# Kernel tuning notes

Hardware: AMD Instinct MI355X
Metric: run time of the kernel (lower is better)

The kernel has to match this reference:

```python
import jax, jax.numpy as jnp
import numpy as np

N, D, E = 16384, 256, 131072  # nodes, feature dim, directed edges (avg sym degree ~16)


def _build_graph(rng):
    # random edges with no self-loops
    r = rng.integers(0, N, E)
    c = (r + 1 + rng.integers(0, N - 1, E)) % N
    e = np.stack([r, c], 1)
    # symmetrize + dedupe + sort == torch sparse coalesce()
    e = np.unique(np.concatenate([e, e[:, ::-1]], 0), axis=0)
    rows, cols = e[:, 0], e[:, 1]
    deg = np.bincount(rows, minlength=N)
    max_deg = int(deg.max())
    off = np.concatenate([[0], np.cumsum(deg)])
    pos = np.arange(rows.shape[0]) - off[rows]
    nbr = np.zeros((N, max_deg), dtype=np.int32)  # padded neighbor lists (CSR rows)
    nbr[rows, pos] = cols
    return nbr, deg.astype(np.int32)


def setup_inputs() -> dict:
    rng = np.random.default_rng(0)
    vertices = jnp.asarray(rng.standard_normal((N, D)).astype(np.float32))
    nbr, deg = _build_graph(rng)
    return {"vertices": vertices, "nbr": jnp.asarray(nbr), "deg": jnp.asarray(deg)}


def _compute_means(vertices, nbr, deg):
    # Sequential greedy edge-based vertex averaging (RelEdgePool phase 1).
    n, d = vertices.shape
    max_deg = nbr.shape[1]
    slot = jnp.arange(max_deg)

    def step(carry, xs):
        unproc, out, c = carry
        i, nbrs_i, deg_i = xs
        valid = slot < deg_i                      # real (non-pad) neighbors
        sel = valid & unproc[nbrs_i]              # unprocessed cluster members (excl. self)
        is_head = unproc[i]                       # vertex starts a new valid cluster
        # mean over unprocessed members; self is always included when head
        s = jnp.einsum('kd,k->d', vertices[nbrs_i], sel.astype(vertices.dtype)) + vertices[i]
        cnt = (jnp.sum(sel) + 1).astype(vertices.dtype)
        mean = s / cnt
        out = out.at[c].set(jnp.where(is_head, mean, out[c]))
        # mark selected members (and self) as processed, only if this is a head
        mark = jnp.zeros(n, bool).at[nbrs_i].max(sel).at[i].set(True)
        unproc = unproc & ~(mark & is_head)
        c = c + is_head.astype(c.dtype)
        return (unproc, out, c), is_head

    init = (jnp.ones(n, dtype=bool), jnp.zeros((n, d), vertices.dtype), jnp.int32(0))
    (_, out, num_clusters), head_mask = jax.lax.scan(
        step, init, (jnp.arange(n), nbr, deg))
    # out[:num_clusters] are the averaged vertices; rows beyond are zero (preallocated buffer,
    # matching the torch code before its final data-dependent slice).
    # head_mask marks vertex_mappings; mean_mappings == arange(num_clusters).
    return out, head_mask, num_clusters


def reference(vertices, nbr, deg):
    return _compute_means(vertices, nbr, deg)
```

## Files before the change

### kernel.cpp

```cpp
#include <hip/hip_runtime.h>
#include <cstdint>
#include <cstddef>

#define NV 16384
#define DD 256
#define TPB 1024
#define BLK 2048
#define PCAP 7
#define HROW 24
#define NPASS 12

#define CFENCE() asm volatile("" ::: "memory")

__global__ __launch_bounds__(256)
void k_prep(const int* __restrict__ nbr, const int* __restrict__ deg,
            int maxdeg, int n, uint4* __restrict__ pend_g,
            unsigned short* __restrict__ hi_g)
{
    int v = blockIdx.x * 256 + threadIdx.x;
    if (v >= n) return;
    const int b  = v & ~(BLK - 1);
    const int dv = deg[v];
    const int* __restrict__ row = nbr + (size_t)v * (size_t)maxdeg;
    unsigned short* __restrict__ hrow = hi_g + (size_t)v * HROW;
    unsigned w0 = 0, w1 = 0, w2 = 0, w3 = 0;
    int cnt = 0, hic = 0;
    for (int k = 0; k < dv; ++k) {
        int j = row[k];
        if (j > v) {
            if (hic < HROW - 1) hrow[1 + hic] = (unsigned short)j;
            ++hic;
        } else if (j >= b) {
            unsigned val = (unsigned)(j - b);
            switch (cnt) {
                case 0: w0 |= val << 16; break;
                case 1: w1 |= val;       break;
                case 2: w1 |= val << 16; break;
                case 3: w2 |= val;       break;
                case 4: w2 |= val << 16; break;
                case 5: w3 |= val;       break;
                case 6: w3 |= val << 16; break;
                default: break;
            }
            ++cnt;
        }
    }
    hrow[0] = (unsigned short)hic;
    w0 |= (unsigned)(cnt > 0xffff ? 0xffff : cnt);
    pend_g[v] = make_uint4(w0, w1, w2, w3);
}

__device__ __forceinline__
void do_push(unsigned char* st, int V,
             const unsigned short* __restrict__ hi_g,
             const int* __restrict__ nbr, const int* __restrict__ deg,
             int maxdeg)
{
    const uint4* hp = (const uint4*)(hi_g + (size_t)V * HROW);
    uint4 H0 = hp[0], H1 = hp[1], H2 = hp[2];
    const int hic = (int)(H0.x & 0xffffu);
    if (hic <= HROW - 1) {
        #define PUSHE(word, sh, k) if ((k) < hic) st[((word) >> (sh)) & 0xffffu] = 2
        PUSHE(H0.x,16, 0); PUSHE(H0.y, 0, 1); PUSHE(H0.y,16, 2);
        PUSHE(H0.z, 0, 3); PUSHE(H0.z,16, 4); PUSHE(H0.w, 0, 5);
        PUSHE(H0.w,16, 6);
        PUSHE(H1.x, 0, 7); PUSHE(H1.x,16, 8); PUSHE(H1.y, 0, 9);
        PUSHE(H1.y,16,10); PUSHE(H1.z, 0,11); PUSHE(H1.z,16,12);
        PUSHE(H1.w, 0,13); PUSHE(H1.w,16,14);
        PUSHE(H2.x, 0,15); PUSHE(H2.x,16,16); PUSHE(H2.y, 0,17);
        PUSHE(H2.y,16,18); PUSHE(H2.z, 0,19); PUSHE(H2.z,16,20);
        PUSHE(H2.w, 0,21); PUSHE(H2.w,16,22);
        #undef PUSHE
    } else {
        const int dv = deg[V];
        const int* __restrict__ row = nbr + (size_t)V * (size_t)maxdeg;
        for (int k = 0; k < dv; ++k) {
            int j = row[k];
            if (j > V) st[j] = 2;
        }
    }
}

__device__ __forceinline__
void decide(int& my, unsigned char* st, int V, int np, int qown,
            int q0, int q1, int q2, int q3, int q4, int q5, int q6, int B,
            const unsigned short* __restrict__ hi_g,
            const int* __restrict__ nbr, const int* __restrict__ deg,
            int maxdeg)
{
    if (qown != 0) { my = 2; return; }
    bool anyH = false; int undec = 0;
    if (np <= PCAP) {
        if (np > 0) { anyH |= (q0 == 1); undec += (q0 == 0); }
        if (np > 1) { anyH |= (q1 == 1); undec += (q1 == 0); }
        if (np > 2) { anyH |= (q2 == 1); undec += (q2 == 0); }
        if (np > 3) { anyH |= (q3 == 1); undec += (q3 == 0); }
        if (np > 4) { anyH |= (q4 == 1); undec += (q4 == 0); }
        if (np > 5) { anyH |= (q5 == 1); undec += (q5 == 0); }
        if (np > 6) { anyH |= (q6 == 1); undec += (q6 == 0); }
    } else {
        const int dv = deg[V];
        const int* __restrict__ row = nbr + (size_t)V * (size_t)maxdeg;
        for (int k = 0; k < dv; ++k) {
            int j = row[k];
            if (j >= B && j < V) {
                int q = st[j];
                anyH |= (q == 1); undec += (q == 0);
            }
        }
    }
    if (anyH) { my = 2; st[V] = 2; }
    else if (undec == 0) {
        my = 1; st[V] = 1;
        do_push(st, V, hi_g, nbr, deg, maxdeg);
    }
}

__global__ __launch_bounds__(TPB, 4)
void k_mis(const int* __restrict__ nbr, const int* __restrict__ deg,
           int maxdeg, int n,
           const uint4* __restrict__ pend_g, const unsigned short* __restrict__ hi_g,
           int* __restrict__ headlist, float* __restrict__ out_tail)
{
    __shared__ __align__(16) unsigned char st[NV];
    __shared__ int s_ws[TPB / 64];
    __shared__ int F[3];
    const int t    = threadIdx.x;
    const int lane = t & 63;
    const int wid  = t >> 6;

    ((uint4*)st)[t] = make_uint4(0u, 0u, 0u, 0u);
    if (t < 3) F[t] = 0;
    __syncthreads();

    uint4 pa0 = make_uint4(0,0,0,0), pa1 = pa0;
    if (t < n)        pa0 = pend_g[t];
    if (1024 + t < n) pa1 = pend_g[1024 + t];
    int r = 0;

    for (int b = 0; b < n; b += BLK) {
        const int v0 = b + t, v1 = b + 1024 + t;
        uint4 qa0 = make_uint4(0,0,0,0), qa1 = qa0;
        {
            int w0 = b + BLK + t, w1 = b + BLK + 1024 + t;
            if (w0 < n) qa0 = pend_g[w0];
            if (w1 < n) qa1 = pend_g[w1];
        }

        const int np0 = pa0.x & 0xffff;
        const int e0 = pa0.x >> 16,    e1 = pa0.y & 0xffff, e2 = pa0.y >> 16;
        const int e3 = pa0.z & 0xffff, e4 = pa0.z >> 16;
        const int e5 = pa0.w & 0xffff, e6 = pa0.w >> 16;
        const int np1 = pa1.x & 0xffff;
        const int f0 = pa1.x >> 16,    f1 = pa1.y & 0xffff, f2 = pa1.y >> 16;
        const int f3 = pa1.z & 0xffff, f4 = pa1.z >> 16;
        const int f5 = pa1.w & 0xffff, f6 = pa1.w >> 16;

        int my0 = (v0 < n) ? 0 : 2;
        int my1 = (v1 < n) ? 0 : 2;

        for (;; ++r) {
            if (t == 0) F[(r + 1) % 3] = 0;
            for (int pass = 0; pass < NPASS; ++pass) {
                int s0  = st[v0 < n ? v0 : 0],  s1  = st[v1 < n ? v1 : 0];
                int q00 = st[b + e0], q01 = st[b + e1], q02 = st[b + e2];
                int q03 = st[b + e3], q04 = st[b + e4], q05 = st[b + e5];
                int q06 = st[b + e6];
                int q10 = st[b + f0], q11 = st[b + f1], q12 = st[b + f2];
                int q13 = st[b + f3], q14 = st[b + f4], q15 = st[b + f5];
                int q16 = st[b + f6];
                if (my0 == 0) decide(my0, st, v0, np0, s0,
                                     q00,q01,q02,q03,q04,q05,q06, b,
                                     hi_g, nbr, deg, maxdeg);
                if (my1 == 0) decide(my1, st, v1, np1, s1,
                                     q10,q11,q12,q13,q14,q15,q16, b,
                                     hi_g, nbr, deg, maxdeg);
                if (__ballot((my0 == 0) || (my1 == 0)) == 0ULL) break;
                CFENCE();
            }
            if ((my0 == 0) || (my1 == 0)) F[r % 3] = 1;
            asm volatile("s_waitcnt lgkmcnt(0)\n\ts_barrier" ::: "memory");
            if (F[r % 3] == 0) { ++r; break; }
        }
        pa0 = qa0; pa1 = qa1;
    }

    uint4 qq = ((const uint4*)st)[t];
    int cnt = __popc(qq.x & 0x01010101u) + __popc(qq.y & 0x01010101u)
            + __popc(qq.z & 0x01010101u) + __popc(qq.w & 0x01010101u);
    int c = cnt;
    #pragma unroll
    for (int off = 1; off < 64; off <<= 1) {
        int x = __shfl_up(c, off);
        if (lane >= off) c += x;
    }
    if (lane == 63) s_ws[wid] = c;
    __syncthreads();
    int wexcl = 0, tot = 0;
    #pragma unroll
    for (int w = 0; w < TPB / 64; ++w) {
        int s = s_ws[w];
        tot += s;
        if (w < wid) wexcl += s;
    }
    int excl = wexcl + (c - cnt);
    #pragma unroll
    for (int i = 0; i < 16; ++i) {
        int v = t * 16 + i;
        if (st[v] == 1) { headlist[excl] = v; ++excl; }
    }
    for (int i = t; i < NV / 4; i += TPB) {
        unsigned w = ((const unsigned*)st)[i];
        float4 f;
        f.x = (float)(w & 1u);         f.y = (float)((w >> 8) & 1u);
        f.z = (float)((w >> 16) & 1u); f.w = (float)((w >> 24) & 1u);
        ((float4*)out_tail)[i] = f;
    }
    if (t == 0) out_tail[n] = (float)tot;
}

__global__ __launch_bounds__(256)
void k_avg(const float* __restrict__ vert, const int* __restrict__ nbr,
           const int* __restrict__ deg, int maxdeg, int n,
           const int* __restrict__ headlist,
           const float* __restrict__ tail, float* __restrict__ out)
{
    const int w    = (blockIdx.x * 256 + threadIdx.x) >> 6;
    const int lane = threadIdx.x & 63;
    if (w >= n) return;
    const int tot  = (int)tail[n];
    if (w >= tot) {
        reinterpret_cast<float4*>(out + (size_t)w * DD)[lane] = make_float4(0.f, 0.f, 0.f, 0.f);
        return;
    }
    const int h = headlist[w];

    const int dh = deg[h];
    const int* __restrict__ row = nbr + (size_t)h * (size_t)maxdeg;

    float4 acc = reinterpret_cast<const float4*>(vert + (size_t)h * DD)[lane];
    int cnt = 1;

    for (int k0 = 0; k0 < dh; k0 += 64) {
        int k = k0 + lane;
        int j = (k < dh) ? row[k] : -1;
        bool mem = false;
        if (j > h && tail[j] == 0.0f) {
            const int dj = deg[j];
            const int* __restrict__ rj = nbr + (size_t)j * (size_t)maxdeg;
            int mn = 0x7fffffff;
            for (int kk = 0; kk < dj; ++kk) {
                int u = rj[kk];
                if (tail[u] != 0.0f) mn = min(mn, u);
            }
            mem = (mn == h);
        }
        unsigned long long m = __ballot(mem);
        cnt += __popcll(m);
        while (m) {
            int bit = __ffsll((long long)m) - 1;
            m &= (m - 1);
            int jj = __shfl(j, bit);
            float4 rr = reinterpret_cast<const float4*>(vert + (size_t)jj * DD)[lane];
            acc.x += rr.x; acc.y += rr.y; acc.z += rr.z; acc.w += rr.w;
        }
    }
    const float inv = 1.0f / (float)cnt;
    float4 res;
    res.x = acc.x * inv; res.y = acc.y * inv;
    res.z = acc.z * inv; res.w = acc.w * inv;
    reinterpret_cast<float4*>(out + (size_t)w * DD)[lane] = res;
}

extern "C" void kernel_launch(void* const* d_in, const int* in_sizes, int n_in,
                              void* d_out, int out_size, void* d_ws, size_t ws_size,
                              hipStream_t stream)
{
    const float* vert = (const float*)d_in[0];
    const int*   nbr  = (const int*)d_in[1];
    const int*   deg  = (const int*)d_in[2];

    const int n      = in_sizes[2];
    const int maxdeg = in_sizes[1] / n;
    const int d      = in_sizes[0] / n;

    int*   headlist = (int*)d_ws;
    uint4* pend_g   = (uint4*)(headlist + n);
    unsigned short* hi_g = (unsigned short*)(pend_g + n);

    float* out      = (float*)d_out;
    float* out_tail = out + (size_t)n * (size_t)d;

    hipLaunchKernelGGL(k_prep, dim3((n + 255) / 256), dim3(256), 0, stream,
                       nbr, deg, maxdeg, n, pend_g, hi_g);

    hipLaunchKernelGGL(k_mis, dim3(1), dim3(TPB), 0, stream,
                       nbr, deg, maxdeg, n, pend_g, hi_g, headlist, out_tail);

    const int blocks = (n * 64 + 255) / 256;
    hipLaunchKernelGGL(k_avg, dim3(blocks), dim3(256), 0, stream,
                       vert, nbr, deg, maxdeg, n, headlist, out_tail, out);
}
```

Before: 87.38 us.

## Replace push-based neighbor marking with pull-based check of earlier-block heads

Heads no longer push a 'covered' mark to their higher-index neighbours. Instead, each vertex pulls at the start of its block: it checks whether any lower-index neighbour from an earlier block is already a head, using packed neighbour lists of up to 23 entries prepared in k_prep. This removes scattered shared-memory writes and the per-head global reads of the hi list from the serial in-block iteration loop. In exchange it adds more register state per thread (three extra uint4 per vertex) and reduces the pass count from 12 to 10.

```diff
diff --git a/kernel.cpp b/kernel.cpp
--- a/kernel.cpp
+++ b/kernel.cpp
@@ -6,91 +6,117 @@
 #define DD 256
 #define TPB 1024
 #define BLK 2048
+#define OCAP 23
 #define PCAP 7
-#define HROW 24
-#define NPASS 12
+#define NPASS 10
 
 #define CFENCE() asm volatile("" ::: "memory")
 
 __global__ __launch_bounds__(256)
 void k_prep(const int* __restrict__ nbr, const int* __restrict__ deg,
-            int maxdeg, int n, uint4* __restrict__ pend_g,
-            unsigned short* __restrict__ hi_g)
+            int maxdeg, int n, uint4* __restrict__ old_g,
+            uint4* __restrict__ pend_g)
 {
     int v = blockIdx.x * 256 + threadIdx.x;
     if (v >= n) return;
-    const int b  = v & ~(BLK - 1);
+    const int B  = v & ~(BLK - 1);
     const int dv = deg[v];
     const int* __restrict__ row = nbr + (size_t)v * (size_t)maxdeg;
-    unsigned short* __restrict__ hrow = hi_g + (size_t)v * HROW;
-    unsigned w0 = 0, w1 = 0, w2 = 0, w3 = 0;
-    int cnt = 0, hic = 0;
+    unsigned o0=0,o1=0,o2=0,o3=0,o4=0,o5=0,o6=0,o7=0,o8=0,o9=0,o10=0,o11=0;
+    unsigned w0=0,w1=0,w2=0,w3=0;
+    int no = 0, np = 0;
     for (int k = 0; k < dv; ++k) {
         int j = row[k];
-        if (j > v) {
-            if (hic < HROW - 1) hrow[1 + hic] = (unsigned short)j;
-            ++hic;
-        } else if (j >= b) {
-            unsigned val = (unsigned)(j - b);
-            switch (cnt) {
-                case 0: w0 |= val << 16; break;
-                case 1: w1 |= val;       break;
-                case 2: w1 |= val << 16; break;
-                case 3: w2 |= val;       break;
-                case 4: w2 |= val << 16; break;
-                case 5: w3 |= val;       break;
-                case 6: w3 |= val << 16; break;
+        if (j >= v) continue;
+        if (j < B) {
+            unsigned e = (unsigned)j;
+            switch (no) {
+                case 0:  o0 |= e << 16; break;
+                case 1:  o1 |= e; break;      case 2:  o1 |= e << 16; break;
+                case 3:  o2 |= e; break;      case 4:  o2 |= e << 16; break;
+                case 5:  o3 |= e; break;      case 6:  o3 |= e << 16; break;
+                case 7:  o4 |= e; break;      case 8:  o4 |= e << 16; break;
+                case 9:  o5 |= e; break;      case 10: o5 |= e << 16; break;
+                case 11: o6 |= e; break;      case 12: o6 |= e << 16; break;
+                case 13: o7 |= e; break;      case 14: o7 |= e << 16; break;
+                case 15: o8 |= e; break;      case 16: o8 |= e << 16; break;
+                case 17: o9 |= e; break;      case 18: o9 |= e << 16; break;
+                case 19: o10 |= e; break;     case 20: o10 |= e << 16; break;
+                case 21: o11 |= e; break;     case 22: o11 |= e << 16; break;
                 default: break;
             }
-            ++cnt;
-        }
-    }
-    hrow[0] = (unsigned short)hic;
-    w0 |= (unsigned)(cnt > 0xffff ? 0xffff : cnt);
+            ++no;
+        } else {
+            unsigned e = (unsigned)(j - B);
+            switch (np) {
+                case 0: w0 |= e << 16; break;
+                case 1: w1 |= e; break;  case 2: w1 |= e << 16; break;
+                case 3: w2 |= e; break;  case 4: w2 |= e << 16; break;
+                case 5: w3 |= e; break;  case 6: w3 |= e << 16; break;
+                default: break;
+            }
+            ++np;
+        }
+    }
+    o0 |= (unsigned)(no > 0xffff ? 0xffff : no);
+    w0 |= (unsigned)(np > 0xffff ? 0xffff : np);
+    old_g[3 * (size_t)v]     = make_uint4(o0, o1, o2, o3);
+    old_g[3 * (size_t)v + 1] = make_uint4(o4, o5, o6, o7);
+    old_g[3 * (size_t)v + 2] = make_uint4(o8, o9, o10, o11);
     pend_g[v] = make_uint4(w0, w1, w2, w3);
 }
 
 __device__ __forceinline__
-void do_push(unsigned char* st, int V,
-             const unsigned short* __restrict__ hi_g,
-             const int* __restrict__ nbr, const int* __restrict__ deg,
-             int maxdeg)
-{
-    const uint4* hp = (const uint4*)(hi_g + (size_t)V * HROW);
-    uint4 H0 = hp[0], H1 = hp[1], H2 = hp[2];
-    const int hic = (int)(H0.x & 0xffffu);
-    if (hic <= HROW - 1) {
-        #define PUSHE(word, sh, k) if ((k) < hic) st[((word) >> (sh)) & 0xffffu] = 2
-        PUSHE(H0.x,16, 0); PUSHE(H0.y, 0, 1); PUSHE(H0.y,16, 2);
-        PUSHE(H0.z, 0, 3); PUSHE(H0.z,16, 4); PUSHE(H0.w, 0, 5);
-        PUSHE(H0.w,16, 6);
-        PUSHE(H1.x, 0, 7); PUSHE(H1.x,16, 8); PUSHE(H1.y, 0, 9);
-        PUSHE(H1.y,16,10); PUSHE(H1.z, 0,11); PUSHE(H1.z,16,12);
-        PUSHE(H1.w, 0,13); PUSHE(H1.w,16,14);
-        PUSHE(H2.x, 0,15); PUSHE(H2.x,16,16); PUSHE(H2.y, 0,17);
-        PUSHE(H2.y,16,18); PUSHE(H2.z, 0,19); PUSHE(H2.z,16,20);
-        PUSHE(H2.w, 0,21); PUSHE(H2.w,16,22);
-        #undef PUSHE
-    } else {
+bool any_old_head(const unsigned char* st, uint4 A, uint4 Bw, uint4 Cw, int no,
+                  int V, int B, const int* __restrict__ nbr,
+                  const int* __restrict__ deg, int maxdeg)
+{
+    if (no > OCAP) {
         const int dv = deg[V];
         const int* __restrict__ row = nbr + (size_t)V * (size_t)maxdeg;
-        for (int k = 0; k < dv; ++k) {
-            int j = row[k];
-            if (j > V) st[j] = 2;
-        }
-    }
+        bool a = false;
+        for (int k = 0; k < dv; ++k) { int j = row[k]; if (j < B) a |= (st[j] == 1); }
+        return a;
+    }
+    bool a;
+    {
+        int q0 = st[A.x >> 16],      q1 = st[A.y & 0xffffu], q2 = st[A.y >> 16];
+        int q3 = st[A.z & 0xffffu],  q4 = st[A.z >> 16],     q5 = st[A.w & 0xffffu];
+        int q6 = st[A.w >> 16],      q7 = st[Bw.x & 0xffffu];
+        a = (no > 0 && q0 == 1) || (no > 1 && q1 == 1) || (no > 2 && q2 == 1)
+         || (no > 3 && q3 == 1) || (no > 4 && q4 == 1) || (no > 5 && q5 == 1)
+         || (no > 6 && q6 == 1) || (no > 7 && q7 == 1);
+    }
+    if (no > 8) {
+        int q8  = st[Bw.x >> 16],     q9  = st[Bw.y & 0xffffu], q10 = st[Bw.y >> 16];
+        int q11 = st[Bw.z & 0xffffu], q12 = st[Bw.z >> 16],     q13 = st[Bw.w & 0xffffu];
+        int q14 = st[Bw.w >> 16],     q15 = st[Cw.x & 0xffffu];
+        a = a || (q8 == 1) || (no > 9 && q9 == 1) || (no > 10 && q10 == 1)
+              || (no > 11 && q11 == 1) || (no > 12 && q12 == 1)
+              || (no > 13 && q13 == 1) || (no > 14 && q14 == 1)
+              || (no > 15 && q15 == 1);
+    }
+    if (no > 16) {
+        int q16 = st[Cw.x >> 16],     q17 = st[Cw.y & 0xffffu], q18 = st[Cw.y >> 16];
+        int q19 = st[Cw.z & 0xffffu], q20 = st[Cw.z >> 16],     q21 = st[Cw.w & 0xffffu];
+        int q22 = st[Cw.w >> 16];
+        a = a || (q16 == 1) || (no > 17 && q17 == 1) || (no > 18 && q18 == 1)
+              || (no > 19 && q19 == 1) || (no > 20 && q20 == 1)
+              || (no > 21 && q21 == 1) || (no > 22 && q22 == 1);
+    }
+    return a;
 }
 
 __device__ __forceinline__
-void decide(int& my, unsigned char* st, int V, int np, int qown,
-            int q0, int q1, int q2, int q3, int q4, int q5, int q6, int B,
-            const unsigned short* __restrict__ hi_g,
-            const int* __restrict__ nbr, const int* __restrict__ deg,
-            int maxdeg)
-{
-    if (qown != 0) { my = 2; return; }
+void pend_decide(int& my, unsigned char* st, int V, int B, uint4 P, int np,
+                 int dvf, const int* __restrict__ nbr, int maxdeg)
+{
     bool anyH = false; int undec = 0;
     if (np <= PCAP) {
+        int q0 = st[B + (P.x >> 16)],      q1 = st[B + (P.y & 0xffffu)];
+        int q2 = st[B + (P.y >> 16)],      q3 = st[B + (P.z & 0xffffu)];
+        int q4 = st[B + (P.z >> 16)],      q5 = st[B + (P.w & 0xffffu)];
+        int q6 = st[B + (P.w >> 16)];
         if (np > 0) { anyH |= (q0 == 1); undec += (q0 == 0); }
         if (np > 1) { anyH |= (q1 == 1); undec += (q1 == 0); }
         if (np > 2) { anyH |= (q2 == 1); undec += (q2 == 0); }
@@ -99,27 +125,20 @@
         if (np > 5) { anyH |= (q5 == 1); undec += (q5 == 0); }
         if (np > 6) { anyH |= (q6 == 1); undec += (q6 == 0); }
     } else {
-        const int dv = deg[V];
         const int* __restrict__ row = nbr + (size_t)V * (size_t)maxdeg;
-        for (int k = 0; k < dv; ++k) {
+        for (int k = 0; k < dvf; ++k) {
             int j = row[k];
-            if (j >= B && j < V) {
-                int q = st[j];
-                anyH |= (q == 1); undec += (q == 0);
-            }
-        }
-    }
-    if (anyH) { my = 2; st[V] = 2; }
-    else if (undec == 0) {
-        my = 1; st[V] = 1;
-        do_push(st, V, hi_g, nbr, deg, maxdeg);
-    }
+            if (j >= B && j < V) { int q = st[j]; anyH |= (q == 1); undec += (q == 0); }
+        }
+    }
+    if (anyH)            { my = 2; st[V] = 2; }
+    else if (undec == 0) { my = 1; st[V] = 1; }
 }
 
 __global__ __launch_bounds__(TPB, 4)
 void k_mis(const int* __restrict__ nbr, const int* __restrict__ deg,
            int maxdeg, int n,
-           const uint4* __restrict__ pend_g, const unsigned short* __restrict__ hi_g,
+           const uint4* __restrict__ old_g, const uint4* __restrict__ pend_g,
            int* __restrict__ headlist, float* __restrict__ out_tail)
 {
     __shared__ __align__(16) unsigned char st[NV];
@@ -133,48 +152,62 @@
     if (t < 3) F[t] = 0;
     __syncthreads();
 
-    uint4 pa0 = make_uint4(0,0,0,0), pa1 = pa0;
-    if (t < n)        pa0 = pend_g[t];
-    if (1024 + t < n) pa1 = pend_g[1024 + t];
+    uint4 a0A = make_uint4(0,0,0,0), a0B = a0A, a0C = a0A, p0 = a0A;
+    uint4 a1A = a0A, a1B = a0A, a1C = a0A, p1 = a0A;
+    {
+        int v0 = t, v1 = 1024 + t;
+        if (v0 < n) {
+            a0A = old_g[3*(size_t)v0]; a0B = old_g[3*(size_t)v0+1];
+            a0C = old_g[3*(size_t)v0+2]; p0 = pend_g[v0];
+        }
+        if (v1 < n) {
+            a1A = old_g[3*(size_t)v1]; a1B = old_g[3*(size_t)v1+1];
+            a1C = old_g[3*(size_t)v1+2]; p1 = pend_g[v1];
+        }
+    }
     int r = 0;
 
     for (int b = 0; b < n; b += BLK) {
         const int v0 = b + t, v1 = b + 1024 + t;
-        uint4 qa0 = make_uint4(0,0,0,0), qa1 = qa0;
+        uint4 s0A = make_uint4(0,0,0,0), s0B = s0A, s0C = s0A, q0 = s0A;
+        uint4 s1A = s0A, s1B = s0A, s1C = s0A, q1 = s0A;
         {
             int w0 = b + BLK + t, w1 = b + BLK + 1024 + t;
-            if (w0 < n) qa0 = pend_g[w0];
-            if (w1 < n) qa1 = pend_g[w1];
-        }
-
-        const int np0 = pa0.x & 0xffff;
-        const int e0 = pa0.x >> 16,    e1 = pa0.y & 0xffff, e2 = pa0.y >> 16;
-        const int e3 = pa0.z & 0xffff, e4 = pa0.z >> 16;
-        const int e5 = pa0.w & 0xffff, e6 = pa0.w >> 16;
-        const int np1 = pa1.x & 0xffff;
-        const int f0 = pa1.x >> 16,    f1 = pa1.y & 0xffff, f2 = pa1.y >> 16;
-        const int f3 = pa1.z & 0xffff, f4 = pa1.z >> 16;
-        const int f5 = pa1.w & 0xffff, f6 = pa1.w >> 16;
+            if (w0 < n) {
+                s0A = old_g[3*(size_t)w0]; s0B = old_g[3*(size_t)w0+1];
+                s0C = old_g[3*(size_t)w0+2]; q0 = pend_g[w0];
+            }
+            if (w1 < n) {
+                s1A = old_g[3*(size_t)w1]; s1B = old_g[3*(size_t)w1+1];
+                s1C = old_g[3*(size_t)w1+2]; q1 = pend_g[w1];
+            }
+        }
+
+        const int no0 = (int)(a0A.x & 0xffffu), np0 = (int)(p0.x & 0xffffu);
+        const int no1 = (int)(a1A.x & 0xffffu), np1 = (int)(p1.x & 0xffffu);
 
         int my0 = (v0 < n) ? 0 : 2;
         int my1 = (v1 < n) ? 0 : 2;
+        int dvf0 = 0, dvf1 = 0;
+        if (my0 == 0 && np0 > PCAP) dvf0 = deg[v0];
+        if (my1 == 0 && np1 > PCAP) dvf1 = deg[v1];
+
+        if (my0 == 0) {
+            bool aH = any_old_head(st, a0A, a0B, a0C, no0, v0, b, nbr, deg, maxdeg);
+            if (aH)            { my0 = 2; st[v0] = 2; }
+            else if (np0 == 0) { my0 = 1; st[v0] = 1; }
+        }
+        if (my1 == 0) {
+            bool aH = any_old_head(st, a1A, a1B, a1C, no1, v1, b, nbr, deg, maxdeg);
+            if (aH)            { my1 = 2; st[v1] = 2; }
+            else if (np1 == 0) { my1 = 1; st[v1] = 1; }
+        }
 
         for (;; ++r) {
             if (t == 0) F[(r + 1) % 3] = 0;
             for (int pass = 0; pass < NPASS; ++pass) {
-                int s0  = st[v0 < n ? v0 : 0],  s1  = st[v1 < n ? v1 : 0];
-                int q00 = st[b + e0], q01 = st[b + e1], q02 = st[b + e2];
-                int q03 = st[b + e3], q04 = st[b + e4], q05 = st[b + e5];
-                int q06 = st[b + e6];
-                int q10 = st[b + f0], q11 = st[b + f1], q12 = st[b + f2];
-                int q13 = st[b + f3], q14 = st[b + f4], q15 = st[b + f5];
-                int q16 = st[b + f6];
-                if (my0 == 0) decide(my0, st, v0, np0, s0,
-                                     q00,q01,q02,q03,q04,q05,q06, b,
-                                     hi_g, nbr, deg, maxdeg);
-                if (my1 == 0) decide(my1, st, v1, np1, s1,
-                                     q10,q11,q12,q13,q14,q15,q16, b,
-                                     hi_g, nbr, deg, maxdeg);
+                if (my0 == 0) pend_decide(my0, st, v0, b, p0, np0, dvf0, nbr, maxdeg);
+                if (my1 == 0) pend_decide(my1, st, v1, b, p1, np1, dvf1, nbr, maxdeg);
                 if (__ballot((my0 == 0) || (my1 == 0)) == 0ULL) break;
                 CFENCE();
             }
@@ -182,7 +215,8 @@
             asm volatile("s_waitcnt lgkmcnt(0)\n\ts_barrier" ::: "memory");
             if (F[r % 3] == 0) { ++r; break; }
         }
-        pa0 = qa0; pa1 = qa1;
+        a0A = s0A; a0B = s0B; a0C = s0C; p0 = q0;
+        a1A = s1A; a1B = s1B; a1C = s1C; p1 = q1;
     }
 
     uint4 qq = ((const uint4*)st)[t];
@@ -286,16 +320,16 @@
 
     int*   headlist = (int*)d_ws;
     uint4* pend_g   = (uint4*)(headlist + n);
-    unsigned short* hi_g = (unsigned short*)(pend_g + n);
+    uint4* old_g    = pend_g + n;
 
     float* out      = (float*)d_out;
     float* out_tail = out + (size_t)n * (size_t)d;
 
     hipLaunchKernelGGL(k_prep, dim3((n + 255) / 256), dim3(256), 0, stream,
-                       nbr, deg, maxdeg, n, pend_g, hi_g);
+                       nbr, deg, maxdeg, n, old_g, pend_g);
 
     hipLaunchKernelGGL(k_mis, dim3(1), dim3(TPB), 0, stream,
-                       nbr, deg, maxdeg, n, pend_g, hi_g, headlist, out_tail);
+                       nbr, deg, maxdeg, n, old_g, pend_g, headlist, out_tail);
 
     const int blocks = (n * 64 + 255) / 256;
     hipLaunchKernelGGL(k_avg, dim3(blocks), dim3(256), 0, stream,
```

After: 97.39 us. 1.11x slower.
